# Kernel tuning notes

Hardware: AMD Instinct MI355X
Metric: run time of the kernel (lower is better)

Reference implementation:

```python
import jax, jax.numpy as jnp
import numpy as np

EPS = 1e-7  # undefined global in source; standard small epsilon
LAMBD_BDC = 1.0
LAMBD_BEC = 1.0
N, C = 8192, 100


def setup_inputs() -> dict:
    key = jax.random.key(0)
    k1, k2 = jax.random.split(key)
    inputs = jax.random.normal(k1, (N, C), dtype=jnp.float32)
    targets = jax.random.randint(k2, (N,), 0, C)
    return {"inputs": inputs, "targets": targets}


def _rest_indices(targets, num_classes):
    # Indices of all classes except the target, preserving original class order
    # (matches torch boolean-mask gather ordering).
    idx = jnp.arange(num_classes)[None, :]                 # [1, C]
    is_target = idx == targets[:, None]                    # [N, C]
    # Stable sort: non-target positions first, in ascending class order.
    order = jnp.argsort(is_target, axis=1, stable=True)    # [N, C]
    return order[:, : num_classes - 1]                     # [N, C-1]


def reference(inputs, targets):
    n, c = inputs.shape
    # Cross-entropy (mean reduction, as nn.CrossEntropyLoss default)
    logp = jax.nn.log_softmax(inputs, axis=1)
    loss_ce = -jnp.mean(jnp.take_along_axis(logp, targets[:, None], axis=1))

    # Gather target logit and the C-1 non-target logits per row
    logits_y = jnp.take_along_axis(inputs, targets[:, None], axis=1)   # [N, 1]
    rest_idx = _rest_indices(targets, c)
    logits_rest = jnp.take_along_axis(inputs, rest_idx, axis=1)        # [N, C-1]

    # BDC: -sum(logsigmoid(y - rest)) / (C-1) / N
    loss_bdc = -jnp.sum(jax.nn.log_sigmoid(logits_y - logits_rest)) / (c - 1) / n

    # BEC: pairwise differences among non-target logits, [N, C-1, C-1]
    diff = logits_rest[:, :, None] - logits_rest[:, None, :]
    loss_bec = -jnp.sum(0.5 * jax.nn.log_sigmoid(diff + EPS)) / (c - 1) / (c - 2) / n

    loss = loss_ce + LAMBD_BDC * loss_bdc + LAMBD_BEC * loss_bec
    return (loss, loss_ce, loss_bdc, loss_bec)
```

## Files before the change

### kernel.cpp

```cpp
#include <hip/hip_runtime.h>

#define NROWS 8192
#define NCLS  100
#define LN2   0.6931471805599453f
#define LOG2E 1.4426950408889634f

#if __has_builtin(__builtin_amdgcn_exp2f)
#define EXP2F(x) __builtin_amdgcn_exp2f(x)
#else
#define EXP2F(x) __expf((x) * LN2)
#endif
#if __has_builtin(__builtin_amdgcn_logf)
#define LOG2F(x) __builtin_amdgcn_logf(x)
#else
#define LOG2F(x) (__logf(x) * LOG2E)
#endif

#define HT(EA, RA, EB, RB, P) { P *= fmaf((EB), (RA), (EA) * (RB)); }

#define TILE16H(Ea, Ra, Eb, Rb, P0, P1, P2, P3) \
  HT(Ea.x, Ra.x, Eb.x, Rb.x, P0) HT(Ea.x, Ra.x, Eb.y, Rb.y, P0) \
  HT(Ea.x, Ra.x, Eb.z, Rb.z, P0) HT(Ea.x, Ra.x, Eb.w, Rb.w, P0) \
  HT(Ea.y, Ra.y, Eb.x, Rb.x, P1) HT(Ea.y, Ra.y, Eb.y, Rb.y, P1) \
  HT(Ea.y, Ra.y, Eb.z, Rb.z, P1) HT(Ea.y, Ra.y, Eb.w, Rb.w, P1) \
  HT(Ea.z, Ra.z, Eb.x, Rb.x, P2) HT(Ea.z, Ra.z, Eb.y, Rb.y, P2) \
  HT(Ea.z, Ra.z, Eb.z, Rb.z, P2) HT(Ea.z, Ra.z, Eb.w, Rb.w, P2) \
  HT(Ea.w, Ra.w, Eb.x, Rb.x, P3) HT(Ea.w, Ra.w, Eb.y, Rb.y, P3) \
  HT(Ea.w, Ra.w, Eb.z, Rb.z, P3) HT(Ea.w, Ra.w, Eb.w, Rb.w, P3)

#define TILEIJ(idx, I, J) \
    float s_##I = sqrtf(fmaf(8.f, (float)(idx), 1.f)); \
    int J = (int)((1.0f + s_##I) * 0.5f); \
    int I = (idx) - ((J * (J - 1)) >> 1);

__global__ __launch_bounds__(256, 8) void cpc_rows(const float* __restrict__ in,
                                                   const int* __restrict__ tgt,
                                                   float* __restrict__ qb) {
    __shared__ __align__(16) float sx[4][128], sE[4][128], sR[4][128];
    __shared__ float bred[4][3];

    const int tid = threadIdx.x;
    const int w   = tid >> 6;
    const int l   = tid & 63;
    const int row = blockIdx.x * 4 + w;
    const float* x = in + row * NCLS;

    float x0 = x[l] * LOG2E;
    float E0 = EXP2F((x0 - 4.f) * 0.5f);
    float R0 = EXP2F((x0 + 4.f) * -0.5f);
    sx[w][l] = x0; sE[w][l] = E0; sR[w][l] = R0;
    const bool v1 = (l < NCLS - 64);
    float x1 = 0.f, E1 = 0.f;
    if (v1) {
        x1 = x[64 + l] * LOG2E;
        E1 = EXP2F((x1 - 4.f) * 0.5f);
        float R1 = EXP2F((x1 + 4.f) * -0.5f);
        sx[w][64 + l] = x1; sE[w][64 + l] = E1; sR[w][64 + l] = R1;
    }
    __syncthreads();

    const int   t  = tgt[row];
    const float xt = sx[w][t];

    float At, Pb, es, xs;
    {
        float a0 = fabsf(xt - x0);
        float e0 = (l == t) ? 0.f : EXP2F(-a0);
        At = a0; Pb = 1.f + e0;
        es = E0 * E0;
        xs = x0;
    }
    {
        float a1 = v1 ? fabsf(xt - x1) : 0.f;
        float e1 = (v1 && (64 + l) != t) ? EXP2F(-fabsf(xt - x1)) : 0.f;
        At += a1; Pb = fmaf(Pb, e1, Pb);
        es = v1 ? fmaf(E1, E1, es) : es;
        xs += x1;
    }
    float lPb = LOG2F(Pb);

    const float* pE = sE[w];
    const float* pR = sR[w];

    float P0 = 1.f, P1 = 1.f, P2 = 1.f, P3 = 1.f;
    float cst = 512.f;
#pragma unroll 1
    for (int it = 0; it < 4; ++it) {
        int idx = it * 64 + l;
        TILEIJ(idx, I, J)
        float4 Ea = *(const float4*)(pE + 4 * I);
        float4 Ra = *(const float4*)(pR + 4 * I);
        float4 Eb = *(const float4*)(pE + 4 * J);
        float4 Rb = *(const float4*)(pR + 4 * J);
        TILE16H(Ea, Ra, Eb, Rb, P0, P1, P2, P3)
    }
    {
        int idx = 256 + l;
        bool tv = idx < 300;
        int idxc = tv ? idx : 0;
        TILEIJ(idxc, I, J)
        float4 Ea = *(const float4*)(pE + 4 * I);
        float4 Ra = *(const float4*)(pR + 4 * I);
        float4 Eb = *(const float4*)(pE + 4 * J);
        float4 Rb = *(const float4*)(pR + 4 * J);
        float S0 = P0, S1 = P1, S2 = P2, S3 = P3;
        TILE16H(Ea, Ra, Eb, Rb, P0, P1, P2, P3)
        P0 = tv ? P0 : S0; P1 = tv ? P1 : S1;
        P2 = tv ? P2 : S2; P3 = tv ? P3 : S3;
        cst += tv ? 128.f : 0.f;
    }
    float Pd0 = 1.f, Pd1 = 1.f;
    {
        bool dv = l < 25;
        int I = dv ? l : 0;
        float4 Ea = *(const float4*)(pE + 4 * I);
        float4 Ra = *(const float4*)(pR + 4 * I);
        TILE16H(Ea, Ra, Ea, Ra, Pd0, Pd1, Pd0, Pd1)
        Pd0 = dv ? Pd0 : 1.f;
        Pd1 = dv ? Pd1 : 1.f;
        cst += dv ? 64.f : 0.f;
    }

    float lS = 2.f * ((LOG2F(P0) + LOG2F(P1)) + (LOG2F(P2) + LOG2F(P3)))
             + LOG2F(Pd0 * Pd1) + cst;

    float r0 = es;
    float rU = xs + At + 2.f * lPb;
    float rW = At + 2.f * lPb - lS;
#pragma unroll
    for (int off = 32; off; off >>= 1) {
        r0 += __shfl_xor(r0, off, 64);
        rU += __shfl_xor(rU, off, 64);
        rW += __shfl_xor(rW, off, 64);
    }
    if (l == 0) {
        bred[w][0] = LN2 * (LOG2F(r0) + 4.f - xt);
        bred[w][1] = LN2 * (50.f * xt - 0.5f * rU);
        bred[w][2] = LN2 * (rW + 1.f);
    }
    __syncthreads();
    if (tid < 3) {
        float s = bred[0][tid] + bred[1][tid] + bred[2][tid] + bred[3][tid];
        qb[tid * (NROWS / 4) + blockIdx.x] = s;
    }
}

__global__ __launch_bounds__(256) void cpc_final(const float* __restrict__ qb,
                                                 float* __restrict__ out) {
    __shared__ double sred[4][3];
    const int tid = threadIdx.x;
    const int lane = tid & 63, wid = tid >> 6;
    const int NB = NROWS / 4;
    double a0 = 0, a1 = 0, a2 = 0;
#pragma unroll
    for (int it = 0; it < 2; ++it) {
        int idx = (it * 256 + tid) * 4;
        float4 v0 = *(const float4*)(qb + idx);
        float4 v1 = *(const float4*)(qb + NB + idx);
        float4 v2 = *(const float4*)(qb + 2 * NB + idx);
        a0 += (double)v0.x; a0 += (double)v0.y; a0 += (double)v0.z; a0 += (double)v0.w;
        a1 += (double)v1.x; a1 += (double)v1.y; a1 += (double)v1.z; a1 += (double)v1.w;
        a2 += (double)v2.x; a2 += (double)v2.y; a2 += (double)v2.z; a2 += (double)v2.w;
    }
#pragma unroll
    for (int off = 32; off; off >>= 1) {
        a0 += __shfl_xor(a0, off, 64);
        a1 += __shfl_xor(a1, off, 64);
        a2 += __shfl_xor(a2, off, 64);
    }
    if (lane == 0) { sred[wid][0] = a0; sred[wid][1] = a1; sred[wid][2] = a2; }
    __syncthreads();
    if (tid == 0) {
        double ce  = (sred[0][0] + sred[1][0] + sred[2][0] + sred[3][0]) / (double)NROWS;
        double bdc = -(sred[0][1] + sred[1][1] + sred[2][1] + sred[3][1])
                     / (double)(NCLS - 1) / (double)NROWS;
        double bec = -0.5 * (sred[0][2] + sred[1][2] + sred[2][2] + sred[3][2])
                     / (double)(NCLS - 1) / (double)(NCLS - 2) / (double)NROWS;
        out[0] = (float)(ce + bdc + bec);
        out[1] = (float)ce;
        out[2] = (float)bdc;
        out[3] = (float)bec;
    }
}

extern "C" void kernel_launch(void* const* d_in, const int* in_sizes, int n_in,
                              void* d_out, int out_size, void* d_ws, size_t ws_size,
                              hipStream_t stream) {
    const float* inputs  = (const float*)d_in[0];
    const int*   targets = (const int*)d_in[1];
    float*       out     = (float*)d_out;
    float*       qb      = (float*)d_ws;

    cpc_rows<<<NROWS / 4, 256, 0, stream>>>(inputs, targets, qb);
    cpc_final<<<1, 256, 0, stream>>>(qb, out);
}
```

Baseline: 15.02 us.

## Fuse final reduction via last-block atomic counter and pack E/R in fp16

```diff
diff --git a/kernel.cpp b/kernel.cpp
--- a/kernel.cpp
+++ b/kernel.cpp
@@ -2,6 +2,7 @@
 
 #define NROWS 8192
 #define NCLS  100
+#define NB    (NROWS / 4)
 #define LN2   0.6931471805599453f
 #define LOG2E 1.4426950408889634f
 
@@ -16,46 +17,64 @@
 #define LOG2F(x) (__logf(x) * LOG2E)
 #endif
 
-#define HT(EA, RA, EB, RB, P) { P *= fmaf((EB), (RA), (EA) * (RB)); }
-
-#define TILE16H(Ea, Ra, Eb, Rb, P0, P1, P2, P3) \
-  HT(Ea.x, Ra.x, Eb.x, Rb.x, P0) HT(Ea.x, Ra.x, Eb.y, Rb.y, P0) \
-  HT(Ea.x, Ra.x, Eb.z, Rb.z, P0) HT(Ea.x, Ra.x, Eb.w, Rb.w, P0) \
-  HT(Ea.y, Ra.y, Eb.x, Rb.x, P1) HT(Ea.y, Ra.y, Eb.y, Rb.y, P1) \
-  HT(Ea.y, Ra.y, Eb.z, Rb.z, P1) HT(Ea.y, Ra.y, Eb.w, Rb.w, P1) \
-  HT(Ea.z, Ra.z, Eb.x, Rb.x, P2) HT(Ea.z, Ra.z, Eb.y, Rb.y, P2) \
-  HT(Ea.z, Ra.z, Eb.z, Rb.z, P2) HT(Ea.z, Ra.z, Eb.w, Rb.w, P2) \
-  HT(Ea.w, Ra.w, Eb.x, Rb.x, P3) HT(Ea.w, Ra.w, Eb.y, Rb.y, P3) \
-  HT(Ea.w, Ra.w, Eb.z, Rb.z, P3) HT(Ea.w, Ra.w, Eb.w, Rb.w, P3)
+typedef _Float16 half8 __attribute__((ext_vector_type(8)));
 
 #define TILEIJ(idx, I, J) \
     float s_##I = sqrtf(fmaf(8.f, (float)(idx), 1.f)); \
     int J = (int)((1.0f + s_##I) * 0.5f); \
     int I = (idx) - ((J * (J - 1)) >> 1);
 
-__global__ __launch_bounds__(256, 8) void cpc_rows(const float* __restrict__ in,
-                                                   const int* __restrict__ tgt,
-                                                   float* __restrict__ qb) {
-    __shared__ __align__(16) float sx[4][128], sE[4][128], sR[4][128];
+#define HT(EA, RA, EB, RB, P) { P *= fmaf((EB), (RA), (EA) * (RB)); }
+
+#define DECLQ(E, R) float E##0, E##1, E##2, E##3, R##0, R##1, R##2, R##3;
+#define LOADQ(ptr, q, E, R) { half8 h_ = (ptr)[q]; \
+    E##0 = (float)h_[0]; E##1 = (float)h_[1]; E##2 = (float)h_[2]; E##3 = (float)h_[3]; \
+    R##0 = (float)h_[4]; R##1 = (float)h_[5]; R##2 = (float)h_[6]; R##3 = (float)h_[7]; }
+
+#define TILE16S(P0, P1, P2, P3) \
+  HT(Ea0, Ra0, Eb0, Rb0, P0) HT(Ea0, Ra0, Eb1, Rb1, P0) \
+  HT(Ea0, Ra0, Eb2, Rb2, P0) HT(Ea0, Ra0, Eb3, Rb3, P0) \
+  HT(Ea1, Ra1, Eb0, Rb0, P1) HT(Ea1, Ra1, Eb1, Rb1, P1) \
+  HT(Ea1, Ra1, Eb2, Rb2, P1) HT(Ea1, Ra1, Eb3, Rb3, P1) \
+  HT(Ea2, Ra2, Eb0, Rb0, P2) HT(Ea2, Ra2, Eb1, Rb1, P2) \
+  HT(Ea2, Ra2, Eb2, Rb2, P2) HT(Ea2, Ra2, Eb3, Rb3, P2) \
+  HT(Ea3, Ra3, Eb0, Rb0, P3) HT(Ea3, Ra3, Eb1, Rb1, P3) \
+  HT(Ea3, Ra3, Eb2, Rb2, P3) HT(Ea3, Ra3, Eb3, Rb3, P3)
+
+__global__ __launch_bounds__(256, 8) void cpc_fused(const float* __restrict__ in,
+                                                    const int* __restrict__ tgt,
+                                                    float* __restrict__ qb,
+                                                    unsigned* __restrict__ cnt,
+                                                    float* __restrict__ out) {
+    __shared__ float sx[4][112];
+    __shared__ __align__(16) _Float16 sq[4][28][8];
     __shared__ float bred[4][3];
+    __shared__ double sred[4][3];
+    __shared__ unsigned lastflag;
 
     const int tid = threadIdx.x;
     const int w   = tid >> 6;
     const int l   = tid & 63;
     const int row = blockIdx.x * 4 + w;
     const float* x = in + row * NCLS;
+    _Float16* hq = (_Float16*)sq[w];
 
     float x0 = x[l] * LOG2E;
-    float E0 = EXP2F((x0 - 4.f) * 0.5f);
-    float R0 = EXP2F((x0 + 4.f) * -0.5f);
-    sx[w][l] = x0; sE[w][l] = E0; sR[w][l] = R0;
+    float E0f = EXP2F((x0 - 4.f) * 0.5f);
+    float R0f = EXP2F((x0 + 4.f) * -0.5f);
+    sx[w][l] = x0;
+    hq[(l >> 2) * 8 + (l & 3)]     = (_Float16)E0f;
+    hq[(l >> 2) * 8 + 4 + (l & 3)] = (_Float16)R0f;
     const bool v1 = (l < NCLS - 64);
-    float x1 = 0.f, E1 = 0.f;
+    float x1 = 0.f, E1f = 0.f;
     if (v1) {
-        x1 = x[64 + l] * LOG2E;
-        E1 = EXP2F((x1 - 4.f) * 0.5f);
-        float R1 = EXP2F((x1 + 4.f) * -0.5f);
-        sx[w][64 + l] = x1; sE[w][64 + l] = E1; sR[w][64 + l] = R1;
+        int c = 64 + l;
+        x1 = x[c] * LOG2E;
+        E1f = EXP2F((x1 - 4.f) * 0.5f);
+        float R1f = EXP2F((x1 + 4.f) * -0.5f);
+        sx[w][c] = x1;
+        hq[(c >> 2) * 8 + (c & 3)]     = (_Float16)E1f;
+        hq[(c >> 2) * 8 + 4 + (c & 3)] = (_Float16)R1f;
     }
     __syncthreads();
 
@@ -67,20 +86,19 @@
         float a0 = fabsf(xt - x0);
         float e0 = (l == t) ? 0.f : EXP2F(-a0);
         At = a0; Pb = 1.f + e0;
-        es = E0 * E0;
+        es = E0f * E0f;
         xs = x0;
     }
     {
         float a1 = v1 ? fabsf(xt - x1) : 0.f;
         float e1 = (v1 && (64 + l) != t) ? EXP2F(-fabsf(xt - x1)) : 0.f;
         At += a1; Pb = fmaf(Pb, e1, Pb);
-        es = v1 ? fmaf(E1, E1, es) : es;
+        es = v1 ? fmaf(E1f, E1f, es) : es;
         xs += x1;
     }
     float lPb = LOG2F(Pb);
 
-    const float* pE = sE[w];
-    const float* pR = sR[w];
+    const half8* pq = (const half8*)sq[w];
 
     float P0 = 1.f, P1 = 1.f, P2 = 1.f, P3 = 1.f;
     float cst = 512.f;
@@ -88,23 +106,21 @@
     for (int it = 0; it < 4; ++it) {
         int idx = it * 64 + l;
         TILEIJ(idx, I, J)
-        float4 Ea = *(const float4*)(pE + 4 * I);
-        float4 Ra = *(const float4*)(pR + 4 * I);
-        float4 Eb = *(const float4*)(pE + 4 * J);
-        float4 Rb = *(const float4*)(pR + 4 * J);
-        TILE16H(Ea, Ra, Eb, Rb, P0, P1, P2, P3)
+        DECLQ(Ea, Ra) DECLQ(Eb, Rb)
+        LOADQ(pq, I, Ea, Ra)
+        LOADQ(pq, J, Eb, Rb)
+        TILE16S(P0, P1, P2, P3)
     }
     {
         int idx = 256 + l;
         bool tv = idx < 300;
         int idxc = tv ? idx : 0;
         TILEIJ(idxc, I, J)
-        float4 Ea = *(const float4*)(pE + 4 * I);
-        float4 Ra = *(const float4*)(pR + 4 * I);
-        float4 Eb = *(const float4*)(pE + 4 * J);
-        float4 Rb = *(const float4*)(pR + 4 * J);
+        DECLQ(Ea, Ra) DECLQ(Eb, Rb)
+        LOADQ(pq, I, Ea, Ra)
+        LOADQ(pq, J, Eb, Rb)
         float S0 = P0, S1 = P1, S2 = P2, S3 = P3;
-        TILE16H(Ea, Ra, Eb, Rb, P0, P1, P2, P3)
+        TILE16S(P0, P1, P2, P3)
         P0 = tv ? P0 : S0; P1 = tv ? P1 : S1;
         P2 = tv ? P2 : S2; P3 = tv ? P3 : S3;
         cst += tv ? 128.f : 0.f;
@@ -113,9 +129,11 @@
     {
         bool dv = l < 25;
         int I = dv ? l : 0;
-        float4 Ea = *(const float4*)(pE + 4 * I);
-        float4 Ra = *(const float4*)(pR + 4 * I);
-        TILE16H(Ea, Ra, Ea, Ra, Pd0, Pd1, Pd0, Pd1)
+        DECLQ(Ea, Ra)
+        LOADQ(pq, I, Ea, Ra)
+        float Eb0 = Ea0, Eb1 = Ea1, Eb2 = Ea2, Eb3 = Ea3;
+        float Rb0 = Ra0, Rb1 = Ra1, Rb2 = Ra2, Rb3 = Ra3;
+        TILE16S(Pd0, Pd1, Pd0, Pd1)
         Pd0 = dv ? Pd0 : 1.f;
         Pd1 = dv ? Pd1 : 1.f;
         cst += dv ? 64.f : 0.f;
@@ -141,45 +159,49 @@
     __syncthreads();
     if (tid < 3) {
         float s = bred[0][tid] + bred[1][tid] + bred[2][tid] + bred[3][tid];
-        qb[tid * (NROWS / 4) + blockIdx.x] = s;
-    }
-}
-
-__global__ __launch_bounds__(256) void cpc_final(const float* __restrict__ qb,
-                                                 float* __restrict__ out) {
-    __shared__ double sred[4][3];
-    const int tid = threadIdx.x;
-    const int lane = tid & 63, wid = tid >> 6;
-    const int NB = NROWS / 4;
-    double a0 = 0, a1 = 0, a2 = 0;
+        qb[tid * NB + blockIdx.x] = s;
+    }
+
+    __syncthreads();
+    if (tid == 0) {
+        __threadfence();
+        unsigned prev = atomicAdd(cnt, 1u);
+        lastflag = (prev == (unsigned)(NB - 1)) ? 1u : 0u;
+    }
+    __syncthreads();
+    if (lastflag) {
+        __threadfence();
+        const int lane = tid & 63, wid = tid >> 6;
+        double a0 = 0, a1 = 0, a2 = 0;
 #pragma unroll
-    for (int it = 0; it < 2; ++it) {
-        int idx = (it * 256 + tid) * 4;
-        float4 v0 = *(const float4*)(qb + idx);
-        float4 v1 = *(const float4*)(qb + NB + idx);
-        float4 v2 = *(const float4*)(qb + 2 * NB + idx);
-        a0 += (double)v0.x; a0 += (double)v0.y; a0 += (double)v0.z; a0 += (double)v0.w;
-        a1 += (double)v1.x; a1 += (double)v1.y; a1 += (double)v1.z; a1 += (double)v1.w;
-        a2 += (double)v2.x; a2 += (double)v2.y; a2 += (double)v2.z; a2 += (double)v2.w;
-    }
+        for (int it = 0; it < 2; ++it) {
+            int idx = (it * 256 + tid) * 4;
+            float4 v0 = *(const float4*)(qb + idx);
+            float4 v1 = *(const float4*)(qb + NB + idx);
+            float4 v2 = *(const float4*)(qb + 2 * NB + idx);
+            a0 += (double)v0.x; a0 += (double)v0.y; a0 += (double)v0.z; a0 += (double)v0.w;
+            a1 += (double)v1.x; a1 += (double)v1.y; a1 += (double)v1.z; a1 += (double)v1.w;
+            a2 += (double)v2.x; a2 += (double)v2.y; a2 += (double)v2.z; a2 += (double)v2.w;
+        }
 #pragma unroll
-    for (int off = 32; off; off >>= 1) {
-        a0 += __shfl_xor(a0, off, 64);
-        a1 += __shfl_xor(a1, off, 64);
-        a2 += __shfl_xor(a2, off, 64);
-    }
-    if (lane == 0) { sred[wid][0] = a0; sred[wid][1] = a1; sred[wid][2] = a2; }
-    __syncthreads();
-    if (tid == 0) {
-        double ce  = (sred[0][0] + sred[1][0] + sred[2][0] + sred[3][0]) / (double)NROWS;
-        double bdc = -(sred[0][1] + sred[1][1] + sred[2][1] + sred[3][1])
-                     / (double)(NCLS - 1) / (double)NROWS;
-        double bec = -0.5 * (sred[0][2] + sred[1][2] + sred[2][2] + sred[3][2])
-                     / (double)(NCLS - 1) / (double)(NCLS - 2) / (double)NROWS;
-        out[0] = (float)(ce + bdc + bec);
-        out[1] = (float)ce;
-        out[2] = (float)bdc;
-        out[3] = (float)bec;
+        for (int off = 32; off; off >>= 1) {
+            a0 += __shfl_xor(a0, off, 64);
+            a1 += __shfl_xor(a1, off, 64);
+            a2 += __shfl_xor(a2, off, 64);
+        }
+        if (lane == 0) { sred[wid][0] = a0; sred[wid][1] = a1; sred[wid][2] = a2; }
+        __syncthreads();
+        if (tid == 0) {
+            double ce  = (sred[0][0] + sred[1][0] + sred[2][0] + sred[3][0]) / (double)NROWS;
+            double bdc = -(sred[0][1] + sred[1][1] + sred[2][1] + sred[3][1])
+                         / (double)(NCLS - 1) / (double)NROWS;
+            double bec = -0.5 * (sred[0][2] + sred[1][2] + sred[2][2] + sred[3][2])
+                         / (double)(NCLS - 1) / (double)(NCLS - 2) / (double)NROWS;
+            out[0] = (float)(ce + bdc + bec);
+            out[1] = (float)ce;
+            out[2] = (float)bdc;
+            out[3] = (float)bec;
+        }
     }
 }
 
@@ -190,7 +212,8 @@
     const int*   targets = (const int*)d_in[1];
     float*       out     = (float*)d_out;
     float*       qb      = (float*)d_ws;
-
-    cpc_rows<<<NROWS / 4, 256, 0, stream>>>(inputs, targets, qb);
-    cpc_final<<<1, 256, 0, stream>>>(qb, out);
+    unsigned*    cnt     = (unsigned*)((char*)d_ws + 32768);
+
+    hipMemsetAsync(cnt, 0, sizeof(unsigned), stream);
+    cpc_fused<<<NB, 256, 0, stream>>>(inputs, targets, qb, cnt, out);
 }
```

After: 52.13 us. +247.0%, slower.
